# Optimization experiments

Measured on AMD Instinct MI355X. Metric: run time of the kernel, lower is better.

The kernel has to match this reference:

```python
import jax, jax.numpy as jnp
import numpy as np

B, C, H, W = 4, 8, 384, 384
CHANS = 18  # MLP hidden width (module default chans=18)
BAND = 32   # half-width of acquired low-frequency band


def setup_inputs() -> dict:
    key = jax.random.key(0)
    ks = jax.random.split(key, 8)
    acquired_kspace = jax.random.normal(ks[0], (B, C, H, W, 2), jnp.float32)
    acquiring_kspace = jax.random.normal(ks[1], (B, C, H, W, 2), jnp.float32)
    mid = W // 2
    am = np.zeros((B, W), np.float32)
    am[:, mid - BAND:mid + BAND] = 1.0  # acquired center band -> left/right well-defined
    acquired_mask = jnp.asarray(am)
    qm = np.zeros((B, W), np.float32)
    qm[:, ::24] = 1.0  # columns currently being acquired
    acquiring_mask = jnp.asarray(qm)
    CH = C * H
    IN = 2 * CH  # concat(acquiring_features, acquired_features)
    # MLP: Linear(IN,CHANS)+ReLU, Linear(CHANS,CHANS)+ReLU x2, Linear(CHANS,1)+Sigmoid (pools=4 layers)
    W1 = jax.random.normal(ks[2], (CHANS, IN), jnp.float32) * 0.02
    b1 = jnp.zeros((CHANS,), jnp.float32)
    W2 = jax.random.normal(ks[3], (CHANS, CHANS), jnp.float32) * 0.02
    b2 = jnp.zeros((CHANS,), jnp.float32)
    W3 = jax.random.normal(ks[4], (CHANS, CHANS), jnp.float32) * 0.02
    b3 = jnp.zeros((CHANS,), jnp.float32)
    W4 = jax.random.normal(ks[5], (1, CHANS), jnp.float32) * 0.02
    b4 = jnp.zeros((1,), jnp.float32)
    return dict(acquired_kspace=acquired_kspace, acquiring_kspace=acquiring_kspace,
                acquired_mask=acquired_mask, acquiring_mask=acquiring_mask,
                W1=W1, b1=b1, W2=W2, b2=b2, W3=W3, b3=b3, W4=W4, b4=b4)


def reference(acquired_kspace, acquiring_kspace, acquired_mask, acquiring_mask,
              W1, b1, W2, b2, W3, b3, W4, b4):
    cabs = lambda x: jnp.sqrt(jnp.sum(x * x, axis=-1))  # complex magnitude of trailing (re,im)
    # per-column flattened features, row-major over (C,H) like torch.flatten: [B, W, C*H]
    Fq = cabs(acquiring_kspace).transpose(0, 3, 1, 2).reshape(B, W, -1)
    Fa = cabs(acquired_kspace).transpose(0, 3, 1, 2).reshape(B, W, -1)
    CH = Fq.shape[-1]
    # split first linear over the concat([acquiring, acquired]) input
    Pq = Fq @ W1[:, :CH].T   # [B, W_i, CHANS]
    Pa = Fa @ W1[:, CH:].T   # [B, W_c, CHANS]
    h = jax.nn.relu(Pq[:, :, None, :] + Pa[:, None, :, :] + b1)  # [B, W_i, W_c, CHANS]
    h = jax.nn.relu(h @ W2.T + b2)
    h = jax.nn.relu(h @ W3.T + b3)
    out = jax.nn.sigmoid(h @ W4.T + b4)[..., 0]  # [B, W_i, W_c]
    # faithful left/right bounds from acquired_mask (same as torch.nonzero(...)[0][0])
    mid = W // 2
    right = mid + jnp.argmax(acquired_mask[:, mid:] < 1.0, axis=1)              # [B]
    left = jnp.argmax(acquired_mask[:, :mid][:, ::-1] < 1.0, axis=1) + 1        # [B]
    c = jnp.arange(W)
    cmask = (c[None, :] >= left[:, None]) & (c[None, :] < right[:, None])       # [B, W_c]
    denom = (right - left).astype(out.dtype)
    heat = jnp.sum(out * cmask[:, None, :].astype(out.dtype), axis=2) / denom[:, None]
    heat = jnp.where(acquiring_mask > 0, heat, jnp.zeros_like(heat))            # only nonzero acquiring cols
    return jnp.broadcast_to(heat[:, None, :], (B, H, W))  # torch.cat of h copies along dim=1
```

## Files before the change

kernel.cpp:

```cpp
#include <hip/hip_runtime.h>
#include <math.h>
#include <limits.h>

#define kB 4
#define kC 8
#define kH 384
#define kW 384
#define kCH (kC * kH)
#define kIN (2 * kCH)
#define kNC 18
#define kMID (kW / 2)

#define NCH 4
#define RPC (kCH / NCH)
#define RSTAGE 192
#define NSTAGE (RPC / RSTAGE)
#define NGRP 48

#define E18(M) M(0) M(1) M(2) M(3) M(4) M(5) M(6) M(7) M(8) M(9) M(10) M(11) M(12) M(13) M(14) M(15) M(16) M(17)

__global__ __launch_bounds__(256)
void proj_kernel(const float* __restrict__ acquired,
                 const float* __restrict__ acquiring,
                 const float* __restrict__ am,
                 const float* __restrict__ qm,
                 const float* __restrict__ W1,
                 float* __restrict__ Pq_part, float* __restrict__ Pa_part) {
    int g = blockIdx.x, chunk = blockIdx.y, b = blockIdx.z;
    int tid = threadIdx.x;
    int w0 = g * 8;
    int r0 = chunk * RPC;

    __shared__ int sL[256], sR[256];
    __shared__ float sQm[8];
    int candR = INT_MAX, candL = INT_MAX;
    for (int i = tid; i < kW - kMID; i += 256)
        if (am[b * kW + kMID + i] < 1.0f) candR = min(candR, i);
    for (int i = tid; i < kMID; i += 256)
        if (am[b * kW + (kMID - 1 - i)] < 1.0f) candL = min(candL, i);
    sL[tid] = candL; sR[tid] = candR;
    if (tid < 8) sQm[tid] = qm[b * kW + w0 + tid];
    __syncthreads();
    for (int s = 128; s > 0; s >>= 1) {
        if (tid < s) {
            sL[tid] = min(sL[tid], sL[tid + s]);
            sR[tid] = min(sR[tid], sR[tid + s]);
        }
        __syncthreads();
    }
    int left  = ((sL[0] == INT_MAX) ? 0 : sL[0]) + 1;
    int right = kMID + ((sR[0] == INT_MAX) ? 0 : sR[0]);

    bool band = (left < w0 + 8) && (right > w0);
    bool acq_any = (sQm[0] > 0.f) || (sQm[1] > 0.f) || (sQm[2] > 0.f) || (sQm[3] > 0.f) ||
                   (sQm[4] > 0.f) || (sQm[5] > 0.f) || (sQm[6] > 0.f) || (sQm[7] > 0.f);
    if (!band && !acq_any) return;

    int c8 = tid & 7, r32 = tid >> 3;
    int w = w0 + c8;
    int lane = tid & 63, wave = tid >> 6;

    __shared__ float sW[RSTAGE][20];
    __shared__ float sRed[4][8][kNC];

    for (int pass = 0; pass < 2; ++pass) {
        bool need = (pass == 0) ? band : acq_any;
        if (!need) continue;
        const float* ks = (pass == 0) ? acquired : acquiring;
        const float* w1 = (pass == 0) ? (W1 + kCH) : W1;

#define PDECL(j) float a##j = 0.0f;
        E18(PDECL)

        for (int st = 0; st < NSTAGE; ++st) {
            int rs = r0 + st * RSTAGE;
            __syncthreads();
            for (int t = tid; t < kNC * RSTAGE; t += 256) {
                int j = t / RSTAGE, i = t - j * RSTAGE;
                sW[i][j] = w1[j * kIN + rs + i];
            }
            __syncthreads();
#pragma unroll
            for (int it = 0; it < RSTAGE / 32; ++it) {
                int rl = r32 + 32 * it;
                const float2 v = *reinterpret_cast<const float2*>(
                    ks + ((size_t)(b * kCH + rs + rl) * kW + w) * 2);
                float f = sqrtf(v.x * v.x + v.y * v.y);
                const float4 q0 = *reinterpret_cast<const float4*>(&sW[rl][0]);
                const float4 q1 = *reinterpret_cast<const float4*>(&sW[rl][4]);
                const float4 q2 = *reinterpret_cast<const float4*>(&sW[rl][8]);
                const float4 q3 = *reinterpret_cast<const float4*>(&sW[rl][12]);
                const float2 q4 = *reinterpret_cast<const float2*>(&sW[rl][16]);
                a0  = fmaf(f, q0.x, a0);  a1  = fmaf(f, q0.y, a1);
                a2  = fmaf(f, q0.z, a2);  a3  = fmaf(f, q0.w, a3);
                a4  = fmaf(f, q1.x, a4);  a5  = fmaf(f, q1.y, a5);
                a6  = fmaf(f, q1.z, a6);  a7  = fmaf(f, q1.w, a7);
                a8  = fmaf(f, q2.x, a8);  a9  = fmaf(f, q2.y, a9);
                a10 = fmaf(f, q2.z, a10); a11 = fmaf(f, q2.w, a11);
                a12 = fmaf(f, q3.x, a12); a13 = fmaf(f, q3.y, a13);
                a14 = fmaf(f, q3.z, a14); a15 = fmaf(f, q3.w, a15);
                a16 = fmaf(f, q4.x, a16); a17 = fmaf(f, q4.y, a17);
            }
        }
#define WRED(j) { a##j += __shfl_down(a##j, 32, 64); a##j += __shfl_down(a##j, 16, 64); \
                  a##j += __shfl_down(a##j, 8, 64); }
        E18(WRED)
        if (lane < 8) {
#define SSTORE(j) sRed[wave][lane][j] = a##j;
            E18(SSTORE)
        }
        __syncthreads();
        if (tid < 8 * kNC) {
            int c = tid / kNC, j = tid - c * kNC;
            float s = sRed[0][c][j] + sRed[1][c][j] + sRed[2][c][j] + sRed[3][c][j];
            float* Pp = (pass == 0) ? Pa_part : Pq_part;
            Pp[(((size_t)chunk * kB + b) * kW + (w0 + c)) * kNC + j] = s;
        }
    }
}

__global__ __launch_bounds__(256)
void pair_kernel(const float* __restrict__ Pq_part, const float* __restrict__ Pa_part,
                 const float* __restrict__ am, const float* __restrict__ qmask,
                 const float* __restrict__ b1, const float* __restrict__ W2,
                 const float* __restrict__ b2, const float* __restrict__ W3,
                 const float* __restrict__ b3, const float* __restrict__ W4,
                 const float* __restrict__ b4, float* __restrict__ heat) {
    int wi = blockIdx.x, b = blockIdx.y, tid = threadIdx.x;
    if (!(qmask[b * kW + wi] > 0.0f)) return;

    __shared__ int sL[256], sR[256];
    int candR = INT_MAX, candL = INT_MAX;
    for (int i = tid; i < kW - kMID; i += 256)
        if (am[b * kW + kMID + i] < 1.0f) candR = min(candR, i);
    for (int i = tid; i < kMID; i += 256)
        if (am[b * kW + (kMID - 1 - i)] < 1.0f) candL = min(candL, i);
    sL[tid] = candL; sR[tid] = candR;
    __syncthreads();
    for (int s = 128; s > 0; s >>= 1) {
        if (tid < s) {
            sL[tid] = min(sL[tid], sL[tid + s]);
            sR[tid] = min(sR[tid], sR[tid + s]);
        }
        __syncthreads();
    }
    int left  = ((sL[0] == INT_MAX) ? 0 : sL[0]) + 1;
    int right = kMID + ((sR[0] == INT_MAX) ? 0 : sR[0]);
    int span = right - left;

    __shared__ float2 sW2[kNC * kNC / 2], sW3[kNC * kNC / 2];
    __shared__ float sW4[kNC], sb1[kNC], sb2[kNC], sb3[kNC], sPq[kNC];
    __shared__ float sb4s, wred[4];
    if (tid < kNC * kNC / 2) {
        sW2[tid] = reinterpret_cast<const float2*>(W2)[tid];
        sW3[tid] = reinterpret_cast<const float2*>(W3)[tid];
    }
    if (tid >= 192 && tid < 192 + kNC) {
        int j = tid - 192;
        float s = 0.0f;
#pragma unroll
        for (int c = 0; c < NCH; ++c)
            s += Pq_part[(((size_t)c * kB + b) * kW + wi) * kNC + j];
        sPq[j] = s;
        sW4[j] = W4[j]; sb1[j] = b1[j]; sb2[j] = b2[j]; sb3[j] = b3[j];
    }
    if (tid == 255) sb4s = b4[0];
    __syncthreads();

#define DOT2(S, k, v) (S[(k)*9+0].x*v##0  + S[(k)*9+0].y*v##1  + \
                       S[(k)*9+1].x*v##2  + S[(k)*9+1].y*v##3  + \
                       S[(k)*9+2].x*v##4  + S[(k)*9+2].y*v##5  + \
                       S[(k)*9+3].x*v##6  + S[(k)*9+3].y*v##7  + \
                       S[(k)*9+4].x*v##8  + S[(k)*9+4].y*v##9  + \
                       S[(k)*9+5].x*v##10 + S[(k)*9+5].y*v##11 + \
                       S[(k)*9+6].x*v##12 + S[(k)*9+6].y*v##13 + \
                       S[(k)*9+7].x*v##14 + S[(k)*9+7].y*v##15 + \
                       S[(k)*9+8].x*v##16 + S[(k)*9+8].y*v##17)

    float ssum = 0.0f;
    for (int wc = left + tid; wc < right; wc += 256) {
        const float* pa0 = Pa_part + (((size_t)0 * kB + b) * kW + wc) * kNC;
        const float* pa1 = Pa_part + (((size_t)1 * kB + b) * kW + wc) * kNC;
        const float* pa2 = Pa_part + (((size_t)2 * kB + b) * kW + wc) * kNC;
        const float* pa3 = Pa_part + (((size_t)3 * kB + b) * kW + wc) * kNC;
#define L1(j) float x##j = fmaxf(sPq[j] + sb1[j] + ((pa0[j] + pa1[j]) + (pa2[j] + pa3[j])), 0.0f);
        E18(L1)
        asm volatile("" ::: "memory");
#define L2(k) float y##k = fmaxf(sb2[k] + DOT2(sW2, k, x), 0.0f);
        E18(L2)
        asm volatile("" ::: "memory");
#define L3(k) float z##k = fmaxf(sb3[k] + DOT2(sW3, k, y), 0.0f);
        E18(L3)
        asm volatile("" ::: "memory");
        float t = sb4s +
            (sW4[0]*z0 + sW4[1]*z1 + sW4[2]*z2 + sW4[3]*z3 + sW4[4]*z4 + sW4[5]*z5 +
             sW4[6]*z6 + sW4[7]*z7 + sW4[8]*z8 + sW4[9]*z9 + sW4[10]*z10 + sW4[11]*z11 +
             sW4[12]*z12 + sW4[13]*z13 + sW4[14]*z14 + sW4[15]*z15 + sW4[16]*z16 + sW4[17]*z17);
        ssum += 1.0f / (1.0f + expf(-t));
    }

    ssum += __shfl_down(ssum, 32, 64); ssum += __shfl_down(ssum, 16, 64);
    ssum += __shfl_down(ssum,  8, 64); ssum += __shfl_down(ssum,  4, 64);
    ssum += __shfl_down(ssum,  2, 64); ssum += __shfl_down(ssum,  1, 64);
    int wave = tid >> 6, lane = tid & 63;
    if (lane == 0) wred[wave] = ssum;
    __syncthreads();
    if (tid == 0)
        heat[b * kW + wi] = (wred[0] + wred[1] + wred[2] + wred[3]) / (float)span;
}

__global__ __launch_bounds__(256)
void out_kernel(const float* __restrict__ heat, const float* __restrict__ qm,
                float* __restrict__ out) {
    int idx = blockIdx.x * 256 + threadIdx.x;
    if (idx >= kB * kH * kW) return;
    int w = idx % kW;
    int b = idx / (kH * kW);
    out[idx] = (qm[b * kW + w] > 0.0f) ? heat[b * kW + w] : 0.0f;
}

extern "C" void kernel_launch(void* const* d_in, const int* in_sizes, int n_in,
                              void* d_out, int out_size, void* d_ws, size_t ws_size,
                              hipStream_t stream) {
    const float* acquired       = (const float*)d_in[0];
    const float* acquiring      = (const float*)d_in[1];
    const float* acquired_mask  = (const float*)d_in[2];
    const float* acquiring_mask = (const float*)d_in[3];
    const float* W1 = (const float*)d_in[4];
    const float* b1 = (const float*)d_in[5];
    const float* W2 = (const float*)d_in[6];
    const float* b2 = (const float*)d_in[7];
    const float* W3 = (const float*)d_in[8];
    const float* b3 = (const float*)d_in[9];
    const float* W4 = (const float*)d_in[10];
    const float* b4 = (const float*)d_in[11];
    float* out = (float*)d_out;

    size_t partN = (size_t)NCH * kB * kW * kNC;
    float* Pa_part = (float*)d_ws;
    float* Pq_part = Pa_part + partN;
    float* heat    = Pq_part + partN;

    proj_kernel<<<dim3(NGRP, NCH, kB), 256, 0, stream>>>(
        acquired, acquiring, acquired_mask, acquiring_mask, W1, Pq_part, Pa_part);
    pair_kernel<<<dim3(kW, kB), 256, 0, stream>>>(
        Pq_part, Pa_part, acquired_mask, acquiring_mask,
        b1, W2, b2, W3, b3, W4, b4, heat);
    int n = kB * kH * kW;
    out_kernel<<<(n + 255) / 256, 256, 0, stream>>>(heat, acquiring_mask, out);
}
```

Baseline: 165.8 us.

## Split projection rows into more chunks, preload k-space, add partial-sum reduce kernel

```diff
diff --git a/kernel.cpp b/kernel.cpp
--- a/kernel.cpp
+++ b/kernel.cpp
@@ -11,13 +11,13 @@
 #define kNC 18
 #define kMID (kW / 2)
 
-#define NCH 4
+#define NCH 8
 #define RPC (kCH / NCH)
-#define RSTAGE 192
-#define NSTAGE (RPC / RSTAGE)
 #define NGRP 48
+#define kN (kB * kW * kNC)
 
 #define E18(M) M(0) M(1) M(2) M(3) M(4) M(5) M(6) M(7) M(8) M(9) M(10) M(11) M(12) M(13) M(14) M(15) M(16) M(17)
+#define E12(M) M(0) M(1) M(2) M(3) M(4) M(5) M(6) M(7) M(8) M(9) M(10) M(11)
 
 __global__ __launch_bounds__(256)
 void proj_kernel(const float* __restrict__ acquired,
@@ -60,7 +60,7 @@
     int w = w0 + c8;
     int lane = tid & 63, wave = tid >> 6;
 
-    __shared__ float sW[RSTAGE][20];
+    __shared__ float sW[RPC][20];
     __shared__ float sRed[4][8][kNC];
 
     for (int pass = 0; pass < 2; ++pass) {
@@ -69,39 +69,41 @@
         const float* ks = (pass == 0) ? acquired : acquiring;
         const float* w1 = (pass == 0) ? (W1 + kCH) : W1;
 
+        const float* colp = ks + ((size_t)(b * kCH + r0 + r32) * kW + w) * 2;
+#define KLOAD(it) const float2 v##it = *reinterpret_cast<const float2*>(colp + (size_t)(it) * 32 * kW * 2);
+        E12(KLOAD)
+#define KMAG(it) const float f##it = sqrtf(v##it.x * v##it.x + v##it.y * v##it.y);
+        E12(KMAG)
+
+        __syncthreads();
+        for (int t = tid; t < kNC * RPC; t += 256) {
+            int j = t / RPC, i = t - j * RPC;
+            sW[i][j] = w1[j * kIN + r0 + i];
+        }
+        __syncthreads();
+
 #define PDECL(j) float a##j = 0.0f;
         E18(PDECL)
 
-        for (int st = 0; st < NSTAGE; ++st) {
-            int rs = r0 + st * RSTAGE;
-            __syncthreads();
-            for (int t = tid; t < kNC * RSTAGE; t += 256) {
-                int j = t / RSTAGE, i = t - j * RSTAGE;
-                sW[i][j] = w1[j * kIN + rs + i];
-            }
-            __syncthreads();
-#pragma unroll
-            for (int it = 0; it < RSTAGE / 32; ++it) {
-                int rl = r32 + 32 * it;
-                const float2 v = *reinterpret_cast<const float2*>(
-                    ks + ((size_t)(b * kCH + rs + rl) * kW + w) * 2);
-                float f = sqrtf(v.x * v.x + v.y * v.y);
-                const float4 q0 = *reinterpret_cast<const float4*>(&sW[rl][0]);
-                const float4 q1 = *reinterpret_cast<const float4*>(&sW[rl][4]);
-                const float4 q2 = *reinterpret_cast<const float4*>(&sW[rl][8]);
-                const float4 q3 = *reinterpret_cast<const float4*>(&sW[rl][12]);
-                const float2 q4 = *reinterpret_cast<const float2*>(&sW[rl][16]);
-                a0  = fmaf(f, q0.x, a0);  a1  = fmaf(f, q0.y, a1);
-                a2  = fmaf(f, q0.z, a2);  a3  = fmaf(f, q0.w, a3);
-                a4  = fmaf(f, q1.x, a4);  a5  = fmaf(f, q1.y, a5);
-                a6  = fmaf(f, q1.z, a6);  a7  = fmaf(f, q1.w, a7);
-                a8  = fmaf(f, q2.x, a8);  a9  = fmaf(f, q2.y, a9);
-                a10 = fmaf(f, q2.z, a10); a11 = fmaf(f, q2.w, a11);
-                a12 = fmaf(f, q3.x, a12); a13 = fmaf(f, q3.y, a13);
-                a14 = fmaf(f, q3.z, a14); a15 = fmaf(f, q3.w, a15);
-                a16 = fmaf(f, q4.x, a16); a17 = fmaf(f, q4.y, a17);
-            }
-        }
+#define ROWF(it) { \
+            const float* row = &sW[r32 + 32 * (it)][0]; \
+            const float4 q0 = *reinterpret_cast<const float4*>(row); \
+            const float4 q1 = *reinterpret_cast<const float4*>(row + 4); \
+            const float4 q2 = *reinterpret_cast<const float4*>(row + 8); \
+            const float4 q3 = *reinterpret_cast<const float4*>(row + 12); \
+            const float2 q4 = *reinterpret_cast<const float2*>(row + 16); \
+            const float f = f##it; \
+            a0  = fmaf(f, q0.x, a0);  a1  = fmaf(f, q0.y, a1);  \
+            a2  = fmaf(f, q0.z, a2);  a3  = fmaf(f, q0.w, a3);  \
+            a4  = fmaf(f, q1.x, a4);  a5  = fmaf(f, q1.y, a5);  \
+            a6  = fmaf(f, q1.z, a6);  a7  = fmaf(f, q1.w, a7);  \
+            a8  = fmaf(f, q2.x, a8);  a9  = fmaf(f, q2.y, a9);  \
+            a10 = fmaf(f, q2.z, a10); a11 = fmaf(f, q2.w, a11); \
+            a12 = fmaf(f, q3.x, a12); a13 = fmaf(f, q3.y, a13); \
+            a14 = fmaf(f, q3.z, a14); a15 = fmaf(f, q3.w, a15); \
+            a16 = fmaf(f, q4.x, a16); a17 = fmaf(f, q4.y, a17); }
+        E12(ROWF)
+
 #define WRED(j) { a##j += __shfl_down(a##j, 32, 64); a##j += __shfl_down(a##j, 16, 64); \
                   a##j += __shfl_down(a##j, 8, 64); }
         E18(WRED)
@@ -114,13 +116,27 @@
             int c = tid / kNC, j = tid - c * kNC;
             float s = sRed[0][c][j] + sRed[1][c][j] + sRed[2][c][j] + sRed[3][c][j];
             float* Pp = (pass == 0) ? Pa_part : Pq_part;
-            Pp[(((size_t)chunk * kB + b) * kW + (w0 + c)) * kNC + j] = s;
-        }
-    }
-}
-
-__global__ __launch_bounds__(256)
-void pair_kernel(const float* __restrict__ Pq_part, const float* __restrict__ Pa_part,
+            Pp[((size_t)chunk * kB * kW + (size_t)b * kW + (w0 + c)) * kNC + j] = s;
+        }
+    }
+}
+
+__global__ __launch_bounds__(256)
+void reduce_kernel(const float* __restrict__ Pa_part, const float* __restrict__ Pq_part,
+                   float* __restrict__ Pa, float* __restrict__ Pq) {
+    int idx = blockIdx.x * 256 + threadIdx.x;
+    if (idx >= 2 * kN) return;
+    const float* src = (idx < kN) ? Pa_part : Pq_part;
+    float* dst = (idx < kN) ? Pa : Pq;
+    int n = (idx < kN) ? idx : idx - kN;
+    float s = 0.0f;
+#pragma unroll
+    for (int c = 0; c < NCH; ++c) s += src[(size_t)c * kN + n];
+    dst[n] = s;
+}
+
+__global__ __launch_bounds__(256)
+void pair_kernel(const float* __restrict__ Pq, const float* __restrict__ Pa,
                  const float* __restrict__ am, const float* __restrict__ qmask,
                  const float* __restrict__ b1, const float* __restrict__ W2,
                  const float* __restrict__ b2, const float* __restrict__ W3,
@@ -157,11 +173,7 @@
     }
     if (tid >= 192 && tid < 192 + kNC) {
         int j = tid - 192;
-        float s = 0.0f;
-#pragma unroll
-        for (int c = 0; c < NCH; ++c)
-            s += Pq_part[(((size_t)c * kB + b) * kW + wi) * kNC + j];
-        sPq[j] = s;
+        sPq[j] = Pq[((size_t)(b * kW + wi)) * kNC + j];
         sW4[j] = W4[j]; sb1[j] = b1[j]; sb2[j] = b2[j]; sb3[j] = b3[j];
     }
     if (tid == 255) sb4s = b4[0];
@@ -179,11 +191,8 @@
 
     float ssum = 0.0f;
     for (int wc = left + tid; wc < right; wc += 256) {
-        const float* pa0 = Pa_part + (((size_t)0 * kB + b) * kW + wc) * kNC;
-        const float* pa1 = Pa_part + (((size_t)1 * kB + b) * kW + wc) * kNC;
-        const float* pa2 = Pa_part + (((size_t)2 * kB + b) * kW + wc) * kNC;
-        const float* pa3 = Pa_part + (((size_t)3 * kB + b) * kW + wc) * kNC;
-#define L1(j) float x##j = fmaxf(sPq[j] + sb1[j] + ((pa0[j] + pa1[j]) + (pa2[j] + pa3[j])), 0.0f);
+        const float* pa = Pa + (size_t)(b * kW + wc) * kNC;
+#define L1(j) float x##j = fmaxf(sPq[j] + sb1[j] + pa[j], 0.0f);
         E18(L1)
         asm volatile("" ::: "memory");
 #define L2(k) float y##k = fmaxf(sb2[k] + DOT2(sW2, k, x), 0.0f);
@@ -236,15 +245,17 @@
     const float* b4 = (const float*)d_in[11];
     float* out = (float*)d_out;
 
-    size_t partN = (size_t)NCH * kB * kW * kNC;
     float* Pa_part = (float*)d_ws;
-    float* Pq_part = Pa_part + partN;
-    float* heat    = Pq_part + partN;
+    float* Pq_part = Pa_part + (size_t)NCH * kN;
+    float* Pa      = Pq_part + (size_t)NCH * kN;
+    float* Pq      = Pa + kN;
+    float* heat    = Pq + kN;
 
     proj_kernel<<<dim3(NGRP, NCH, kB), 256, 0, stream>>>(
         acquired, acquiring, acquired_mask, acquiring_mask, W1, Pq_part, Pa_part);
+    reduce_kernel<<<(2 * kN + 255) / 256, 256, 0, stream>>>(Pa_part, Pq_part, Pa, Pq);
     pair_kernel<<<dim3(kW, kB), 256, 0, stream>>>(
-        Pq_part, Pa_part, acquired_mask, acquiring_mask,
+        Pq, Pa, acquired_mask, acquiring_mask,
         b1, W2, b2, W3, b3, W4, b4, heat);
     int n = kB * kH * kW;
     out_kernel<<<(n + 255) / 256, 256, 0, stream>>>(heat, acquiring_mask, out);
```

New measurement: 148.7 us. 1.12x faster.
